# Kernel optimization log

Measured on AMD Instinct MI355X. Metric: run time of the kernel, lower is better.

The kernel has to match this reference:

```python
import jax, jax.numpy as jnp
import numpy as np

B, S, D = 4, 8192, 1024

def log_g(x):
    # log of g(x): log(x + 0.5) for x >= 0, log(sigmoid(x)) = -softplus(-x) otherwise
    return jnp.where(x >= 0, jnp.log(jax.nn.relu(x) + 0.5), -jax.nn.softplus(-x))

def setup_inputs() -> dict:
    key = jax.random.key(0)
    k1, k2 = jax.random.split(key)
    x = jax.random.normal(k1, (B, S, D), dtype=jnp.float32)
    # Linear(dim, 3*dim, bias=False); stored as [dim, 3*dim] so y = x @ W
    W = jax.random.normal(k2, (D, 3 * D), dtype=jnp.float32) * (1.0 / np.sqrt(D))
    return {"x": x, "W": W}

def reference(x, W):
    # x: [B, S, D], W: [D, 3D]
    hW = jnp.einsum('bsd,de->bse', x, W)  # [B, S, 3D]
    hidden, f_gate, i_gate = jnp.split(hW, 3, axis=-1)

    # log-space normalized gates:
    # diff = softplus(-f) - softplus(-i); log_f' = -softplus(diff); log_i' = -softplus(-diff)
    diff = jax.nn.softplus(-f_gate) - jax.nn.softplus(-i_gate)
    log_f = -jax.nn.softplus(diff)
    log_i = -jax.nn.softplus(-diff)
    log_values = log_i + log_g(hidden)

    # Heinsen associative scan in log space (float32 internally)
    a_star = jnp.cumsum(log_f.astype(jnp.float32), axis=1)
    log_h0_plus_b_star = jax.lax.cumlogsumexp(log_values.astype(jnp.float32) - a_star, axis=1)
    log_h = a_star + log_h0_plus_b_star
    out = jnp.exp(log_h).astype(x.dtype)  # [B, S, D]
    return out
```

## Files before the change

kernel.cpp:

```cpp
#include <hip/hip_runtime.h>
#include <hip/hip_bf16.h>
#include <cstdint>
#include <cstddef>


#define BB 4
#define SS 8192
#define DD 1024
#define MM 32768
#define KK 1024
#define NN 3072
#define CHUNKS 256
#define CLEN 32
#define NCH 4096
#define NT 16

typedef __bf16 bf16;
typedef __bf16 bf16x2 __attribute__((ext_vector_type(2)));
typedef __bf16 bf16x4 __attribute__((ext_vector_type(4)));
typedef __bf16 bf16x8 __attribute__((ext_vector_type(8)));
typedef float f32x4 __attribute__((ext_vector_type(4)));

__device__ __forceinline__ void gload16(const bf16* g, bf16* l) {
  __builtin_amdgcn_global_load_lds(
      (const __attribute__((address_space(1))) unsigned int*)(const void*)g,
      (__attribute__((address_space(3))) unsigned int*)(void*)l,
      16, 0, 0);
}

__device__ __forceinline__ float sp(float x) {
  return fmaxf(x, 0.f) + __logf(1.f + __expf(-fabsf(x)));
}
__device__ __forceinline__ void gates(float h, float f, float i,
                                      float& lf, float& lv) {
  float d = sp(-f) - sp(-i);
  float spd = sp(d);
  lf = -spd;
  float li = d - spd;
  float lg = (h >= 0.f) ? __logf(h + 0.5f) : -sp(-h);
  lv = li + lg;
}
__device__ __forceinline__ float laddexp(float a, float b) {
  float m = fmaxf(a, b);
  return m + __logf(1.f + __expf(fminf(a, b) - m));
}
__device__ __forceinline__ void comb(float& A, float& V, float Ac, float Vc) {
  V = laddexp(V + Ac, Vc);
  A += Ac;
}

__global__ __launch_bounds__(256) void k_cvt_x(const float4* __restrict__ x,
                                               bf16x4* __restrict__ xb) {
  int i = blockIdx.x * 256 + threadIdx.x;
  float4 v = x[i];
  bf16x4 o;
  o[0] = (bf16)v.x; o[1] = (bf16)v.y; o[2] = (bf16)v.z; o[3] = (bf16)v.w;
  xb[i] = o;
}

__global__ __launch_bounds__(256) void k_cvt_wt(const float* __restrict__ W,
                                                bf16* __restrict__ Wt) {
  __shared__ float tile[32][33];
  int n0 = blockIdx.x * 32, k0 = blockIdx.y * 32;
  int tx = threadIdx.x, ty = threadIdx.y;
#pragma unroll
  for (int i = 0; i < 32; i += 8)
    tile[ty + i][tx] = W[(size_t)(k0 + ty + i) * NN + n0 + tx];
  __syncthreads();
#pragma unroll
  for (int i = 0; i < 32; i += 8)
    Wt[(size_t)(n0 + ty + i) * KK + k0 + tx] = (bf16)tile[tx][ty + i];
}

__global__ __launch_bounds__(512, 2) void k_gemm(const bf16* __restrict__ A,
                                                 const bf16* __restrict__ Bt,
                                                 bf16* __restrict__ C) {
  __shared__ __align__(16) bf16 sm[65536];
  const int tid = threadIdx.x;
  const int lane = tid & 63;
  const int w = tid >> 6;
  const int wm = w >> 2;
  const int wn = w & 3;
  const int c16 = lane & 15;
  const int l4 = lane >> 4;

  int bid = blockIdx.x;
  int swz = (bid & 7) * 192 + (bid >> 3);
  int mT = swz / 12;
  int nT = swz - mT * 12;
  const int mBase = mT * 256, nBase = nT * 256;

  const int sr = tid >> 3;
  const int scol = ((tid & 7) ^ (sr & 7)) * 8;
  const bf16* gA = A + (size_t)(mBase + sr) * KK + scol;
  const bf16* gB = Bt + (size_t)(nBase + sr) * KK + scol;
  const int ld = tid * 8;

  const int sw8 = c16 & 7;
  const int sx0 = (l4 ^ sw8) * 8;
  const int sx1 = ((l4 + 4) ^ sw8) * 8;
  const int aRow = (wm * 64 + c16) * 64;
  const int bRow = (wn * 32 + c16) * 64;

  f32x4 acc[2][2][4][2];
#pragma unroll
  for (int a = 0; a < 2; ++a)
#pragma unroll
    for (int b2 = 0; b2 < 2; ++b2)
#pragma unroll
      for (int m = 0; m < 4; ++m)
#pragma unroll
        for (int n = 0; n < 2; ++n)
          acc[a][b2][m][n] = (f32x4){0.f, 0.f, 0.f, 0.f};

#define STGA(h, L, bo, ko) \
  gload16(gA + (h) * 131072 + (L) * 65536 + (ko), \
          sm + (bo) + (h) * 8192 + (L) * 4096 + ld)
#define STGB(h, L, bo, ko) \
  gload16(gB + (h) * 131072 + (L) * 65536 + (ko), \
          sm + (bo) + 16384 + (h) * 8192 + (L) * 4096 + ld)
#define LDA(qm)                                                         \
  _Pragma("unroll") for (int mi = 0; mi < 4; ++mi) {                    \
    const bf16* p_ = sm + buf + (qm) * 8192 + aRow + mi * 1024;         \
    afr[mi][0] = *(const bf16x8*)(p_ + sx0);                            \
    afr[mi][1] = *(const bf16x8*)(p_ + sx1);                            \
  }
#define LDB(qn)                                                         \
  _Pragma("unroll") for (int ni = 0; ni < 2; ++ni) {                    \
    const bf16* p_ = sm + buf + 16384 + (qn) * 8192 + bRow + ni * 1024; \
    bfr[ni][0] = *(const bf16x8*)(p_ + sx0);                            \
    bfr[ni][1] = *(const bf16x8*)(p_ + sx1);                            \
  }
#define MFMAQ(qm, qn)                                                     \
  __builtin_amdgcn_s_setprio(1);                                          \
  _Pragma("unroll") for (int mi = 0; mi < 4; ++mi)                        \
  _Pragma("unroll") for (int ni = 0; ni < 2; ++ni) {                      \
    acc[qm][qn][mi][ni] = __builtin_amdgcn_mfma_f32_16x16x32_bf16(        \
        afr[mi][0], bfr[ni][0], acc[qm][qn][mi][ni], 0, 0, 0);            \
    acc[qm][qn][mi][ni] = __builtin_amdgcn_mfma_f32_16x16x32_bf16(        \
        afr[mi][1], bfr[ni][1], acc[qm][qn][mi][ni], 0, 0, 0);            \
  }                                                                       \
  __builtin_amdgcn_s_setprio(0);
#define BAR asm volatile("s_barrier" ::: "memory")
#define VMC(n) asm volatile("s_waitcnt vmcnt(" #n ")" ::: "memory")

  STGA(0, 0, 0, 0); STGA(0, 1, 0, 0); STGB(0, 0, 0, 0); STGB(0, 1, 0, 0);
  STGA(1, 0, 0, 0); STGA(1, 1, 0, 0); STGB(1, 0, 0, 0); STGB(1, 1, 0, 0);
  VMC(4);
  BAR;

  bf16x8 afr[4][2], bfr[2][2];

  for (int t = 0; t < NT - 1; ++t) {
    const int buf = (t & 1) << 15;
    const int nb = buf ^ 32768;
    const int ko = (t + 1) * 64;
    LDA(0); LDB(0);
    STGA(0, 0, nb, ko); STGA(0, 1, nb, ko);
    STGB(0, 0, nb, ko); STGB(0, 1, nb, ko);
    VMC(4);
    BAR;
    MFMAQ(0, 0);
    BAR;
    LDA(1);
    STGA(1, 0, nb, ko); STGA(1, 1, nb, ko);
    BAR;
    MFMAQ(1, 0);
    BAR;
    LDB(1);
    STGB(1, 0, nb, ko); STGB(1, 1, nb, ko);
    BAR;
    MFMAQ(1, 1);
    BAR;
    LDA(0);
    VMC(4);
    BAR;
    MFMAQ(0, 1);
    BAR;
  }
  {
    const int buf = 32768;
    LDA(0); LDB(0);
    VMC(0);
    BAR;
    MFMAQ(0, 0);
    BAR;
    LDA(1);
    BAR;
    MFMAQ(1, 0);
    BAR;
    LDB(1);
    BAR;
    MFMAQ(1, 1);
    BAR;
    LDA(0);
    BAR;
    MFMAQ(0, 1);
  }

  __syncthreads();
  const int rq = l4 * 4;
#pragma unroll
  for (int qm = 0; qm < 2; ++qm)
#pragma unroll
    for (int qn = 0; qn < 2; ++qn)
#pragma unroll
      for (int mi = 0; mi < 4; ++mi)
#pragma unroll
        for (int ni = 0; ni < 2; ++ni)
#pragma unroll
          for (int r = 0; r < 4; ++r) {
            int row = qm * 128 + wm * 64 + mi * 16 + rq + r;
            int col = (qn * 128 + wn * 32 + ni * 16 + c16) ^ ((row & 7) << 3);
            sm[row * 256 + col] = (bf16)acc[qm][qn][mi][ni][r];
          }
  __syncthreads();
#pragma unroll
  for (int p = 0; p < 16; ++p) {
    int row = p * 16 + (tid >> 5);
    int colL = (tid & 31) * 8;
    int col = colL ^ ((row & 7) << 3);
    bf16x8 v = *(const bf16x8*)(sm + row * 256 + col);
    *(bf16x8*)(C + (size_t)(mBase + row) * NN + nBase + colL) = v;
  }
#undef STGA
#undef STGB
#undef LDA
#undef LDB
#undef MFMAQ
#undef BAR
#undef VMC
}

__global__ __launch_bounds__(256, 6) void k_scan1(const bf16* __restrict__ hW,
                                                  float2* __restrict__ agg) {
  const int d0 = (blockIdx.x * 256 + threadIdx.x) * 2;
  const int b = blockIdx.y, c = blockIdx.z;
  const bf16* p = hW + (size_t)(b * SS + c * CLEN) * NN + d0;
  float A0 = 0.f, V0 = -1e30f, A1 = 0.f, V1 = -1e30f;
  bf16x2 hh = *(const bf16x2*)(p);
  bf16x2 ff = *(const bf16x2*)(p + DD);
  bf16x2 ii = *(const bf16x2*)(p + 2 * DD);
#pragma unroll 4
  for (int j = 0; j < CLEN - 1; ++j) {
    p += NN;
    bf16x2 hn = *(const bf16x2*)(p);
    bf16x2 fn = *(const bf16x2*)(p + DD);
    bf16x2 in2 = *(const bf16x2*)(p + 2 * DD);
    float lf, lv;
    gates((float)hh[0], (float)ff[0], (float)ii[0], lf, lv);
    A0 += lf; V0 = laddexp(V0 + lf, lv);
    gates((float)hh[1], (float)ff[1], (float)ii[1], lf, lv);
    A1 += lf; V1 = laddexp(V1 + lf, lv);
    hh = hn; ff = fn; ii = in2;
  }
  float lf, lv;
  gates((float)hh[0], (float)ff[0], (float)ii[0], lf, lv);
  A0 += lf; V0 = laddexp(V0 + lf, lv);
  gates((float)hh[1], (float)ff[1], (float)ii[1], lf, lv);
  A1 += lf; V1 = laddexp(V1 + lf, lv);
  const size_t ch = (size_t)b * DD + d0;
  agg[ch * CHUNKS + c] = make_float2(A0, V0);
  agg[(ch + 1) * CHUNKS + c] = make_float2(A1, V1);
}

__global__ __launch_bounds__(256) void k_scan2(const float2* __restrict__ agg,
                                               float2* __restrict__ pre) {
  const int ch = blockIdx.x * 4 + (threadIdx.x >> 6);
  const int lane = threadIdx.x & 63;
  const float4* src = (const float4*)(agg + (size_t)ch * CHUNKS);
  float4 v0 = src[lane * 2];
  float4 v1 = src[lane * 2 + 1];
  float A = v0.x, V = v0.y;
  comb(A, V, v0.z, v0.w);
  comb(A, V, v1.x, v1.y);
  comb(A, V, v1.z, v1.w);
#pragma unroll
  for (int off = 1; off < 64; off <<= 1) {
    float Ao = __shfl_up(A, off);
    float Vo = __shfl_up(V, off);
    if (lane >= off) {
      V = laddexp(Vo + A, V);
      A = Ao + A;
    }
  }
  float exA = __shfl_up(A, 1);
  float exV = __shfl_up(V, 1);
  if (lane == 0) { exA = 0.f; exV = -1e30f; }
  float4 o0, o1;
  o0.x = exA; o0.y = exV;
  comb(exA, exV, v0.x, v0.y);
  o0.z = exA; o0.w = exV;
  comb(exA, exV, v0.z, v0.w);
  o1.x = exA; o1.y = exV;
  comb(exA, exV, v1.x, v1.y);
  o1.z = exA; o1.w = exV;
  float4* dst = (float4*)(pre + (size_t)ch * CHUNKS);
  dst[lane * 2] = o0;
  dst[lane * 2 + 1] = o1;
}

__global__ __launch_bounds__(256, 6) void k_scan3(const bf16* __restrict__ hW,
                                                  const float2* __restrict__ pre,
                                                  float* __restrict__ out) {
  const int d0 = (blockIdx.x * 256 + threadIdx.x) * 2;
  const int b = blockIdx.y, c = blockIdx.z;
  const bf16* p = hW + (size_t)(b * SS + c * CLEN) * NN + d0;
  float* o = out + (size_t)(b * SS + c * CLEN) * DD + d0;
  const size_t ch = (size_t)b * DD + d0;
  float V0 = pre[ch * CHUNKS + c].y;
  float V1 = pre[(ch + 1) * CHUNKS + c].y;
  bf16x2 hh = *(const bf16x2*)(p);
  bf16x2 ff = *(const bf16x2*)(p + DD);
  bf16x2 ii = *(const bf16x2*)(p + 2 * DD);
#pragma unroll 4
  for (int j = 0; j < CLEN - 1; ++j) {
    p += NN;
    bf16x2 hn = *(const bf16x2*)(p);
    bf16x2 fn = *(const bf16x2*)(p + DD);
    bf16x2 in2 = *(const bf16x2*)(p + 2 * DD);
    float lf, lv;
    gates((float)hh[0], (float)ff[0], (float)ii[0], lf, lv);
    V0 = laddexp(V0 + lf, lv);
    gates((float)hh[1], (float)ff[1], (float)ii[1], lf, lv);
    V1 = laddexp(V1 + lf, lv);
    *(float2*)o = make_float2(__expf(V0), __expf(V1));
    o += DD;
    hh = hn; ff = fn; ii = in2;
  }
  float lf, lv;
  gates((float)hh[0], (float)ff[0], (float)ii[0], lf, lv);
  V0 = laddexp(V0 + lf, lv);
  gates((float)hh[1], (float)ff[1], (float)ii[1], lf, lv);
  V1 = laddexp(V1 + lf, lv);
  *(float2*)o = make_float2(__expf(V0), __expf(V1));
}

extern "C" void kernel_launch(void* const* d_in, const int* in_sizes, int n_in,
                              void* d_out, int out_size, void* d_ws,
                              size_t ws_size, hipStream_t stream) {
  const float* x = (const float*)d_in[0];
  const float* W = (const float*)d_in[1];
  float* out = (float*)d_out;
  char* ws = (char*)d_ws;

  const size_t wtB = (size_t)NN * KK * 2;
  const size_t xbB = (size_t)MM * KK * 2;
  const size_t aggB = (size_t)CHUNKS * NCH * sizeof(float2);
  bf16* Wt = (bf16*)ws;
  bf16* xb = (bf16*)(ws + wtB);
  bf16* hW = (bf16*)(ws + wtB + xbB);
  float2* agg = (float2*)(ws + wtB);
  float2* pre = (float2*)(ws + wtB + aggB);

  k_cvt_wt<<<dim3(NN / 32, KK / 32), dim3(32, 8), 0, stream>>>(W, Wt);
  k_cvt_x<<<dim3(MM * KK / 4 / 256), dim3(256), 0, stream>>>((const float4*)x,
                                                             (bf16x4*)xb);
  k_gemm<<<dim3((NN / 256) * (MM / 256)), dim3(512), 0, stream>>>(xb, Wt, hW);
  k_scan1<<<dim3(DD / 512, BB, CHUNKS), 256, 0, stream>>>(hW, agg);
  k_scan2<<<dim3(NCH / 4), 256, 0, stream>>>(agg, pre);
  k_scan3<<<dim3(DD / 512, BB, CHUNKS), 256, 0, stream>>>(hW, pre, out);
}
```

Baseline: 624.4 us.

## Run chunk scans in linear space with closed-form gates; reorder GEMM quadrant schedule

The per-element gate math is rewritten in linear space: forget and input-times-g weights come from a few exps and reciprocals, replacing several log/softplus evaluations. Within each chunk the recurrence becomes a plain FMA product, converted to log only at chunk boundaries. The scan kernels now handle four channels per thread with vector loads and stores, using fewer blocks. The GEMM inner loop is reordered with a second B-fragment register set so one LDS A reload per iteration is removed. Linear-space accumulation can underflow or overflow within a chunk, which the clamps only partly guard against.

```diff
diff --git a/kernel.cpp b/kernel.cpp
--- a/kernel.cpp
+++ b/kernel.cpp
@@ -28,18 +28,17 @@
       16, 0, 0);
 }
 
-__device__ __forceinline__ float sp(float x) {
-  return fmaxf(x, 0.f) + __logf(1.f + __expf(-fabsf(x)));
-}
-__device__ __forceinline__ void gates(float h, float f, float i,
-                                      float& lf, float& lv) {
-  float d = sp(-f) - sp(-i);
-  float spd = sp(d);
-  lf = -spd;
-  float li = d - spd;
-  float lg = (h >= 0.f) ? __logf(h + 0.5f) : -sp(-h);
-  lv = li + lg;
-}
+__device__ __forceinline__ void gate2(float h, float f, float i,
+                                      float& F, float& IG) {
+  float P = __expf(fminf(-f, 80.f));
+  float Q = __expf(fminf(-i, 80.f));
+  float rZ = __builtin_amdgcn_rcpf(2.f + P + Q);
+  float eh = __expf(fminf(-h, 80.f));
+  float gh = (h >= 0.f) ? (h + 0.5f) : __builtin_amdgcn_rcpf(1.f + eh);
+  F = (1.f + Q) * rZ;
+  IG = (1.f + P) * gh * rZ;
+}
+
 __device__ __forceinline__ float laddexp(float a, float b) {
   float m = fmaxf(a, b);
   return m + __logf(1.f + __expf(fminf(a, b) - m));
@@ -119,26 +118,26 @@
 #define STGB(h, L, bo, ko) \
   gload16(gB + (h) * 131072 + (L) * 65536 + (ko), \
           sm + (bo) + 16384 + (h) * 8192 + (L) * 4096 + ld)
-#define LDA(qm)                                                         \
+#define LDA(qm, AF)                                                     \
   _Pragma("unroll") for (int mi = 0; mi < 4; ++mi) {                    \
     const bf16* p_ = sm + buf + (qm) * 8192 + aRow + mi * 1024;         \
-    afr[mi][0] = *(const bf16x8*)(p_ + sx0);                            \
-    afr[mi][1] = *(const bf16x8*)(p_ + sx1);                            \
-  }
-#define LDB(qn)                                                         \
+    AF[mi][0] = *(const bf16x8*)(p_ + sx0);                             \
+    AF[mi][1] = *(const bf16x8*)(p_ + sx1);                             \
+  }
+#define LDB(qn, BF)                                                     \
   _Pragma("unroll") for (int ni = 0; ni < 2; ++ni) {                    \
     const bf16* p_ = sm + buf + 16384 + (qn) * 8192 + bRow + ni * 1024; \
-    bfr[ni][0] = *(const bf16x8*)(p_ + sx0);                            \
-    bfr[ni][1] = *(const bf16x8*)(p_ + sx1);                            \
-  }
-#define MFMAQ(qm, qn)                                                     \
+    BF[ni][0] = *(const bf16x8*)(p_ + sx0);                             \
+    BF[ni][1] = *(const bf16x8*)(p_ + sx1);                             \
+  }
+#define MFMAQ(qm, qn, AF, BF)                                             \
   __builtin_amdgcn_s_setprio(1);                                          \
   _Pragma("unroll") for (int mi = 0; mi < 4; ++mi)                        \
   _Pragma("unroll") for (int ni = 0; ni < 2; ++ni) {                      \
     acc[qm][qn][mi][ni] = __builtin_amdgcn_mfma_f32_16x16x32_bf16(        \
-        afr[mi][0], bfr[ni][0], acc[qm][qn][mi][ni], 0, 0, 0);            \
+        AF[mi][0], BF[ni][0], acc[qm][qn][mi][ni], 0, 0, 0);              \
     acc[qm][qn][mi][ni] = __builtin_amdgcn_mfma_f32_16x16x32_bf16(        \
-        afr[mi][1], bfr[ni][1], acc[qm][qn][mi][ni], 0, 0, 0);            \
+        AF[mi][1], BF[ni][1], acc[qm][qn][mi][ni], 0, 0, 0);              \
   }                                                                       \
   __builtin_amdgcn_s_setprio(0);
 #define BAR asm volatile("s_barrier" ::: "memory")
@@ -149,53 +148,50 @@
   VMC(4);
   BAR;
 
-  bf16x8 afr[4][2], bfr[2][2];
+  bf16x8 afr[4][2], bfr0[2][2], bfr1[2][2];
 
   for (int t = 0; t < NT - 1; ++t) {
     const int buf = (t & 1) << 15;
     const int nb = buf ^ 32768;
     const int ko = (t + 1) * 64;
-    LDA(0); LDB(0);
+    LDA(0, afr); LDB(0, bfr0);
     STGA(0, 0, nb, ko); STGA(0, 1, nb, ko);
     STGB(0, 0, nb, ko); STGB(0, 1, nb, ko);
     VMC(4);
     BAR;
-    MFMAQ(0, 0);
-    BAR;
-    LDA(1);
+    MFMAQ(0, 0, afr, bfr0);
+    BAR;
+    LDB(1, bfr1);
     STGA(1, 0, nb, ko); STGA(1, 1, nb, ko);
     BAR;
-    MFMAQ(1, 0);
-    BAR;
-    LDB(1);
+    MFMAQ(0, 1, afr, bfr1);
+    BAR;
+    LDA(1, afr);
     STGB(1, 0, nb, ko); STGB(1, 1, nb, ko);
     BAR;
-    MFMAQ(1, 1);
-    BAR;
-    LDA(0);
+    MFMAQ(1, 1, afr, bfr1);
+    BAR;
     VMC(4);
     BAR;
-    MFMAQ(0, 1);
+    MFMAQ(1, 0, afr, bfr0);
     BAR;
   }
   {
     const int buf = 32768;
-    LDA(0); LDB(0);
+    LDA(0, afr); LDB(0, bfr0);
     VMC(0);
     BAR;
-    MFMAQ(0, 0);
-    BAR;
-    LDA(1);
-    BAR;
-    MFMAQ(1, 0);
-    BAR;
-    LDB(1);
-    BAR;
-    MFMAQ(1, 1);
-    BAR;
-    LDA(0);
-    BAR;
-    MFMAQ(0, 1);
+    MFMAQ(0, 0, afr, bfr0);
+    BAR;
+    LDB(1, bfr1);
+    BAR;
+    MFMAQ(0, 1, afr, bfr1);
+    BAR;
+    LDA(1, afr);
+    BAR;
+    MFMAQ(1, 1, afr, bfr1);
+    BAR;
+    MFMAQ(1, 0, afr, bfr0);
   }
 
   __syncthreads();
@@ -234,34 +230,41 @@
 
 __global__ __launch_bounds__(256, 6) void k_scan1(const bf16* __restrict__ hW,
                                                   float2* __restrict__ agg) {
-  const int d0 = (blockIdx.x * 256 + threadIdx.x) * 2;
+  const int d0 = threadIdx.x * 4;
   const int b = blockIdx.y, c = blockIdx.z;
   const bf16* p = hW + (size_t)(b * SS + c * CLEN) * NN + d0;
-  float A0 = 0.f, V0 = -1e30f, A1 = 0.f, V1 = -1e30f;
-  bf16x2 hh = *(const bf16x2*)(p);
-  bf16x2 ff = *(const bf16x2*)(p + DD);
-  bf16x2 ii = *(const bf16x2*)(p + 2 * DD);
+  float Fp[4] = {1.f, 1.f, 1.f, 1.f};
+  float v[4] = {0.f, 0.f, 0.f, 0.f};
+  bf16x4 hh = *(const bf16x4*)(p);
+  bf16x4 ff = *(const bf16x4*)(p + DD);
+  bf16x4 ii = *(const bf16x4*)(p + 2 * DD);
 #pragma unroll 4
   for (int j = 0; j < CLEN - 1; ++j) {
     p += NN;
-    bf16x2 hn = *(const bf16x2*)(p);
-    bf16x2 fn = *(const bf16x2*)(p + DD);
-    bf16x2 in2 = *(const bf16x2*)(p + 2 * DD);
-    float lf, lv;
-    gates((float)hh[0], (float)ff[0], (float)ii[0], lf, lv);
-    A0 += lf; V0 = laddexp(V0 + lf, lv);
-    gates((float)hh[1], (float)ff[1], (float)ii[1], lf, lv);
-    A1 += lf; V1 = laddexp(V1 + lf, lv);
+    bf16x4 hn = *(const bf16x4*)(p);
+    bf16x4 fn = *(const bf16x4*)(p + DD);
+    bf16x4 in2 = *(const bf16x4*)(p + 2 * DD);
+#pragma unroll
+    for (int e = 0; e < 4; ++e) {
+      float F, IG;
+      gate2((float)hh[e], (float)ff[e], (float)ii[e], F, IG);
+      v[e] = fmaf(v[e], F, IG);
+      Fp[e] *= F;
+    }
     hh = hn; ff = fn; ii = in2;
   }
-  float lf, lv;
-  gates((float)hh[0], (float)ff[0], (float)ii[0], lf, lv);
-  A0 += lf; V0 = laddexp(V0 + lf, lv);
-  gates((float)hh[1], (float)ff[1], (float)ii[1], lf, lv);
-  A1 += lf; V1 = laddexp(V1 + lf, lv);
+#pragma unroll
+  for (int e = 0; e < 4; ++e) {
+    float F, IG;
+    gate2((float)hh[e], (float)ff[e], (float)ii[e], F, IG);
+    v[e] = fmaf(v[e], F, IG);
+    Fp[e] *= F;
+  }
   const size_t ch = (size_t)b * DD + d0;
-  agg[ch * CHUNKS + c] = make_float2(A0, V0);
-  agg[(ch + 1) * CHUNKS + c] = make_float2(A1, V1);
+#pragma unroll
+  for (int e = 0; e < 4; ++e)
+    agg[(ch + e) * CHUNKS + c] =
+        make_float2(__logf(fmaxf(Fp[e], 1e-37f)), __logf(fmaxf(v[e], 1e-37f)));
 }
 
 __global__ __launch_bounds__(256) void k_scan2(const float2* __restrict__ agg,
@@ -303,37 +306,45 @@
 __global__ __launch_bounds__(256, 6) void k_scan3(const bf16* __restrict__ hW,
                                                   const float2* __restrict__ pre,
                                                   float* __restrict__ out) {
-  const int d0 = (blockIdx.x * 256 + threadIdx.x) * 2;
+  const int d0 = threadIdx.x * 4;
   const int b = blockIdx.y, c = blockIdx.z;
   const bf16* p = hW + (size_t)(b * SS + c * CLEN) * NN + d0;
   float* o = out + (size_t)(b * SS + c * CLEN) * DD + d0;
   const size_t ch = (size_t)b * DD + d0;
-  float V0 = pre[ch * CHUNKS + c].y;
-  float V1 = pre[(ch + 1) * CHUNKS + c].y;
-  bf16x2 hh = *(const bf16x2*)(p);
-  bf16x2 ff = *(const bf16x2*)(p + DD);
-  bf16x2 ii = *(const bf16x2*)(p + 2 * DD);
+  float v[4];
+#pragma unroll
+  for (int e = 0; e < 4; ++e)
+    v[e] = __expf(pre[(ch + e) * CHUNKS + c].y);
+  bf16x4 hh = *(const bf16x4*)(p);
+  bf16x4 ff = *(const bf16x4*)(p + DD);
+  bf16x4 ii = *(const bf16x4*)(p + 2 * DD);
 #pragma unroll 4
   for (int j = 0; j < CLEN - 1; ++j) {
     p += NN;
-    bf16x2 hn = *(const bf16x2*)(p);
-    bf16x2 fn = *(const bf16x2*)(p + DD);
-    bf16x2 in2 = *(const bf16x2*)(p + 2 * DD);
-    float lf, lv;
-    gates((float)hh[0], (float)ff[0], (float)ii[0], lf, lv);
-    V0 = laddexp(V0 + lf, lv);
-    gates((float)hh[1], (float)ff[1], (float)ii[1], lf, lv);
-    V1 = laddexp(V1 + lf, lv);
-    *(float2*)o = make_float2(__expf(V0), __expf(V1));
+    bf16x4 hn = *(const bf16x4*)(p);
+    bf16x4 fn = *(const bf16x4*)(p + DD);
+    bf16x4 in2 = *(const bf16x4*)(p + 2 * DD);
+    float4 ov;
+#pragma unroll
+    for (int e = 0; e < 4; ++e) {
+      float F, IG;
+      gate2((float)hh[e], (float)ff[e], (float)ii[e], F, IG);
+      v[e] = fmaf(v[e], F, IG);
+    }
+    ov.x = v[0]; ov.y = v[1]; ov.z = v[2]; ov.w = v[3];
+    *(float4*)o = ov;
     o += DD;
     hh = hn; ff = fn; ii = in2;
   }
-  float lf, lv;
-  gates((float)hh[0], (float)ff[0], (float)ii[0], lf, lv);
-  V0 = laddexp(V0 + lf, lv);
-  gates((float)hh[1], (float)ff[1], (float)ii[1], lf, lv);
-  V1 = laddexp(V1 + lf, lv);
-  *(float2*)o = make_float2(__expf(V0), __expf(V1));
+  float4 ov;
+#pragma unroll
+  for (int e = 0; e < 4; ++e) {
+    float F, IG;
+    gate2((float)hh[e], (float)ff[e], (float)ii[e], F, IG);
+    v[e] = fmaf(v[e], F, IG);
+  }
+  ov.x = v[0]; ov.y = v[1]; ov.z = v[2]; ov.w = v[3];
+  *(float4*)o = ov;
 }
 
 extern "C" void kernel_launch(void* const* d_in, const int* in_sizes, int n_in,
@@ -356,8 +367,8 @@
   k_cvt_wt<<<dim3(NN / 32, KK / 32), dim3(32, 8), 0, stream>>>(W, Wt);
   k_cvt_x<<<dim3(MM * KK / 4 / 256), dim3(256), 0, stream>>>((const float4*)x,
                                                              (bf16x4*)xb);
-  k_gemm<<<dim3((NN / 256) * (MM / 256)), dim3(512), 0, stream>>>(xb, Wt, hW);
-  k_scan1<<<dim3(DD / 512, BB, CHUNKS), 256, 0, stream>>>(hW, agg);
+  k_gemm<<<dim3((NN / 256) * (MM / 256)), 512, 0, stream>>>(xb, Wt, hW);
+  k_scan1<<<dim3(1, BB, CHUNKS), 256, 0, stream>>>(hW, agg);
   k_scan2<<<dim3(NCH / 4), 256, 0, stream>>>(agg, pre);
-  k_scan3<<<dim3(DD / 512, BB, CHUNKS), 256, 0, stream>>>(hW, pre, out);
-}
+  k_scan3<<<dim3(1, BB, CHUNKS), 256, 0, stream>>>(hW, pre, out);
+}
```

Measured after the change: 533.6 us. -14.5%, faster.
